# Kernel tuning notes

Hardware: AMD Instinct MI355X
Metric: run time of the kernel (lower is better)

## Reference

```python
import jax, jax.numpy as jnp
import numpy as np

N = 50000   # nodes
E = 800000  # edges (avg degree 16)
D = 96      # feature dim for all layers


def setup_inputs() -> dict:
    key = jax.random.key(0)
    ks = jax.random.split(key, 8)
    x = jax.random.normal(ks[0], (N, D), dtype=jnp.float32)
    edge_index = jax.random.randint(ks[1], (2, E), 0, N, dtype=jnp.int32)
    edge_weight = jax.random.uniform(ks[2], (E,), dtype=jnp.float32)
    batch = jnp.zeros((N,), dtype=jnp.int32)  # unused by forward, kept for signature fidelity
    s = 1.0 / np.sqrt(D)
    W1 = jax.random.normal(ks[3], (D, D), dtype=jnp.float32) * s
    b1 = jnp.zeros((D,), dtype=jnp.float32)
    W2 = jax.random.normal(ks[4], (D, D), dtype=jnp.float32) * s
    b2 = jnp.zeros((D,), dtype=jnp.float32)
    return {"x": x, "edge_index": edge_index, "edge_weight": edge_weight,
            "batch": batch, "W1": W1, "b1": b1, "W2": W2, "b2": b2}


def gcn_conv(x, row, col, ew, W, b):
    """PyG GCNConv: add self-loops (weight 1), symmetric normalization,
    linear transform then weighted scatter-add aggregation at target (col)."""
    n = x.shape[0]
    h = x @ W  # [N, D_out]
    # degree includes self-loop weight 1.0
    deg = jax.ops.segment_sum(ew, col, num_segments=n) + 1.0
    dinv = jnp.where(deg > 0, jax.lax.rsqrt(deg), 0.0)
    norm = dinv[row] * ew * dinv[col]                      # [E]
    agg = jax.ops.segment_sum(h[row] * norm[:, None], col, num_segments=n)
    agg = agg + h * (dinv * dinv)[:, None]                 # self-loop messages
    return agg + b


def reference(x, edge_index, edge_weight, batch, W1, b1, W2, b2):
    row, col = edge_index[0], edge_index[1]
    # layer 1: conv -> relu (dropout p=0.0 is a no-op)
    h = jax.nn.relu(gcn_conv(x, row, col, edge_weight, W1, b1))
    # layer 2
    h = jax.nn.relu(gcn_conv(h, row, col, edge_weight, W2, b2))
    return h
```

## Files before the change

### kernel.cpp

```cpp
#include <hip/hip_runtime.h>
#include <hip/hip_fp16.h>

#define DIM 96
#define DIM4 (DIM/4)
#define CAP 64

typedef _Float16 f16x8 __attribute__((ext_vector_type(8)));
typedef float    f32x4 __attribute__((ext_vector_type(4)));

#define WSCALE 4194304.0f


#define PREP_BLOCKS 256

__global__ __launch_bounds__(256) void prep_kernel(unsigned long long* __restrict__ pdeg,
                                                   const float* __restrict__ W1,
                                                   const float* __restrict__ W2,
                                                   _Float16* __restrict__ Bt1,
                                                   _Float16* __restrict__ Bt2, int n) {
    for (int i = blockIdx.x * 256 + threadIdx.x; i < n; i += PREP_BLOCKS * 256)
        pdeg[i] = 0ULL;
    int i = blockIdx.x * 256 + threadIdx.x;
    if (i < DIM * DIM) {
        int c = i / DIM, k = i - c * DIM;
        Bt1[i] = (_Float16)W1[k * DIM + c];
        Bt2[i] = (_Float16)W2[k * DIM + c];
    }
}


__global__ void edge_pack_kernel(const int* __restrict__ col, const float* __restrict__ ew,
                                 unsigned long long* __restrict__ pdeg,
                                 unsigned* __restrict__ spack,
                                 const int* __restrict__ row, int e) {
    int i = blockIdx.x * blockDim.x + threadIdx.x;
    if (i < e) {
        float w = ew[i];
        unsigned q = (unsigned)(w * WSCALE + 0.5f);
        unsigned long long old =
            atomicAdd(&pdeg[col[i]], (1ULL << 32) | (unsigned long long)q);
        unsigned rk = (unsigned)(old >> 32);
        if (rk < CAP) {
            unsigned hb = (unsigned)__half_as_ushort(__float2half_rn(w));
            spack[(size_t)col[i] * CAP + rk] = ((unsigned)row[i] << 16) | hb;
        }
    }
}


__global__ void dinv_kernel(const unsigned long long* __restrict__ pdeg,
                            float* __restrict__ dinv, int* __restrict__ cnt, int n) {
    int i = blockIdx.x * blockDim.x + threadIdx.x;
    if (i < n) {
        unsigned long long p = pdeg[i];
        int c = (int)(p >> 32);
        cnt[i] = c > CAP ? CAP : c;
        float deg = 1.0f + (float)(p & 0xffffffffULL) * (1.0f / WSCALE);
        dinv[i] = rsqrtf(deg);
    }
}


template<bool A_IS_F32>
__global__ __launch_bounds__(256) void gemm_mfma_kernel(const void* __restrict__ Av,
                                                        const _Float16* __restrict__ Bt,
                                                        const float* __restrict__ dinv,
                                                        _Float16* __restrict__ H, int n) {
    int wave = threadIdx.x >> 6;
    int lane = threadIdx.x & 63;
    int r0 = blockIdx.x * 64 + wave * 16;
    if (r0 >= n) return;

    int lrow = lane & 15;
    int lk   = (lane >> 4) << 3;
    int arow = r0 + lrow;
    if (arow > n - 1) arow = n - 1;

    const _Float16* Ah = (const _Float16*)Av;
    const float*    Af = (const float*)Av;

    f32x4 acc[6] = {};

#pragma unroll
    for (int ks = 0; ks < 3; ++ks) {
        int k0 = ks * 32 + lk;
        f16x8 a;
        if (A_IS_F32) {
            const float* ap = Af + (size_t)arow * DIM + k0;
            float4 x0 = *(const float4*)ap;
            float4 x1 = *(const float4*)(ap + 4);
            a[0] = (_Float16)x0.x; a[1] = (_Float16)x0.y;
            a[2] = (_Float16)x0.z; a[3] = (_Float16)x0.w;
            a[4] = (_Float16)x1.x; a[5] = (_Float16)x1.y;
            a[6] = (_Float16)x1.z; a[7] = (_Float16)x1.w;
        } else {
            a = *(const f16x8*)(Ah + (size_t)arow * DIM + k0);
        }
#pragma unroll
        for (int ct = 0; ct < 6; ++ct) {
            f16x8 b = *(const f16x8*)(Bt + (size_t)(ct * 16 + lrow) * DIM + k0);
            acc[ct] = __builtin_amdgcn_mfma_f32_16x16x32_f16(a, b, acc[ct], 0, 0, 0);
        }
    }

    int crow = r0 + ((lane >> 4) << 2);
    int ccol = lane & 15;
#pragma unroll
    for (int ct = 0; ct < 6; ++ct) {
#pragma unroll
        for (int j = 0; j < 4; ++j) {
            int rr = crow + j;
            if (rr < n)
                H[(size_t)rr * DIM + ct * 16 + ccol] = (_Float16)(acc[ct][j] * dinv[rr]);
        }
    }
}


#define GLN 12
#define GNPB 16

__device__ __forceinline__ float4 half4_to_float4_u2(unsigned a, unsigned b) {
    __half2 h01 = *(const __half2*)&a;
    __half2 h23 = *(const __half2*)&b;
    float2 f01 = __half22float2(h01);
    float2 f23 = __half22float2(h23);
    return make_float4(f01.x, f01.y, f23.x, f23.y);
}

__device__ __forceinline__ float wdec(unsigned e) {
    return __half2float(__ushort_as_half((unsigned short)(e & 0xffffu)));
}

template<bool OUT_F32>
__global__ __launch_bounds__(192) void gather_kernel(const int* __restrict__ cnt,
                                                     const unsigned* __restrict__ spack,
                                                     const float* __restrict__ dinv,
                                                     const __half* __restrict__ H,
                                                     const float* __restrict__ bias,
                                                     float* __restrict__ outf,
                                                     __half* __restrict__ outh, int n) {
    int ln = threadIdx.x / GLN;
    int q  = threadIdx.x - ln * GLN;
    int node = blockIdx.x * GNPB + ln;
    if (node >= n) return;

    const unsigned* seg = spack + (size_t)node * CAP;
    int nedge = cnt[node];
    float di = dinv[node];

    const uint4* Hq = (const uint4*)H;

    float4 accA = make_float4(0.f, 0.f, 0.f, 0.f);
    float4 accB = make_float4(0.f, 0.f, 0.f, 0.f);
    int p = 0;
    for (; p + 3 < nedge; p += 4) {
        unsigned e0 = seg[p];
        unsigned e1 = seg[p + 1];
        unsigned e2 = seg[p + 2];
        unsigned e3 = seg[p + 3];
        uint4 v0 = Hq[(e0 >> 16) * 12 + q];
        uint4 v1 = Hq[(e1 >> 16) * 12 + q];
        uint4 v2 = Hq[(e2 >> 16) * 12 + q];
        uint4 v3 = Hq[(e3 >> 16) * 12 + q];
        float w0 = wdec(e0), w1 = wdec(e1), w2 = wdec(e2), w3 = wdec(e3);
        float4 a0 = half4_to_float4_u2(v0.x, v0.y), b0 = half4_to_float4_u2(v0.z, v0.w);
        float4 a1 = half4_to_float4_u2(v1.x, v1.y), b1 = half4_to_float4_u2(v1.z, v1.w);
        float4 a2 = half4_to_float4_u2(v2.x, v2.y), b2 = half4_to_float4_u2(v2.z, v2.w);
        float4 a3 = half4_to_float4_u2(v3.x, v3.y), b3 = half4_to_float4_u2(v3.z, v3.w);
        accA.x = fmaf(w0, a0.x, accA.x); accA.y = fmaf(w0, a0.y, accA.y);
        accA.z = fmaf(w0, a0.z, accA.z); accA.w = fmaf(w0, a0.w, accA.w);
        accB.x = fmaf(w0, b0.x, accB.x); accB.y = fmaf(w0, b0.y, accB.y);
        accB.z = fmaf(w0, b0.z, accB.z); accB.w = fmaf(w0, b0.w, accB.w);
        accA.x = fmaf(w1, a1.x, accA.x); accA.y = fmaf(w1, a1.y, accA.y);
        accA.z = fmaf(w1, a1.z, accA.z); accA.w = fmaf(w1, a1.w, accA.w);
        accB.x = fmaf(w1, b1.x, accB.x); accB.y = fmaf(w1, b1.y, accB.y);
        accB.z = fmaf(w1, b1.z, accB.z); accB.w = fmaf(w1, b1.w, accB.w);
        accA.x = fmaf(w2, a2.x, accA.x); accA.y = fmaf(w2, a2.y, accA.y);
        accA.z = fmaf(w2, a2.z, accA.z); accA.w = fmaf(w2, a2.w, accA.w);
        accB.x = fmaf(w2, b2.x, accB.x); accB.y = fmaf(w2, b2.y, accB.y);
        accB.z = fmaf(w2, b2.z, accB.z); accB.w = fmaf(w2, b2.w, accB.w);
        accA.x = fmaf(w3, a3.x, accA.x); accA.y = fmaf(w3, a3.y, accA.y);
        accA.z = fmaf(w3, a3.z, accA.z); accA.w = fmaf(w3, a3.w, accA.w);
        accB.x = fmaf(w3, b3.x, accB.x); accB.y = fmaf(w3, b3.y, accB.y);
        accB.z = fmaf(w3, b3.z, accB.z); accB.w = fmaf(w3, b3.w, accB.w);
    }
    for (; p < nedge; ++p) {
        unsigned e0 = seg[p];
        float w0 = wdec(e0);
        uint4 v0 = Hq[(e0 >> 16) * 12 + q];
        float4 a0 = half4_to_float4_u2(v0.x, v0.y), b0 = half4_to_float4_u2(v0.z, v0.w);
        accA.x = fmaf(w0, a0.x, accA.x); accA.y = fmaf(w0, a0.y, accA.y);
        accA.z = fmaf(w0, a0.z, accA.z); accA.w = fmaf(w0, a0.w, accA.w);
        accB.x = fmaf(w0, b0.x, accB.x); accB.y = fmaf(w0, b0.y, accB.y);
        accB.z = fmaf(w0, b0.z, accB.z); accB.w = fmaf(w0, b0.w, accB.w);
    }

    uint4 hv = Hq[node * 12 + q];
    float4 hcA = half4_to_float4_u2(hv.x, hv.y);
    float4 hcB = half4_to_float4_u2(hv.z, hv.w);
    float4 bA = ((const float4*)bias)[2 * q];
    float4 bB = ((const float4*)bias)[2 * q + 1];

    float4 oA, oB;
    oA.x = fmaxf(fmaf(accA.x + hcA.x, di, bA.x), 0.0f);
    oA.y = fmaxf(fmaf(accA.y + hcA.y, di, bA.y), 0.0f);
    oA.z = fmaxf(fmaf(accA.z + hcA.z, di, bA.z), 0.0f);
    oA.w = fmaxf(fmaf(accA.w + hcA.w, di, bA.w), 0.0f);
    oB.x = fmaxf(fmaf(accB.x + hcB.x, di, bB.x), 0.0f);
    oB.y = fmaxf(fmaf(accB.y + hcB.y, di, bB.y), 0.0f);
    oB.z = fmaxf(fmaf(accB.z + hcB.z, di, bB.z), 0.0f);
    oB.w = fmaxf(fmaf(accB.w + hcB.w, di, bB.w), 0.0f);

    if (OUT_F32) {
        ((float4*)(outf + (size_t)node * DIM))[2 * q]     = oA;
        ((float4*)(outf + (size_t)node * DIM))[2 * q + 1] = oB;
    } else {
        __half2 p01 = __float22half2_rn(make_float2(oA.x, oA.y));
        __half2 p23 = __float22half2_rn(make_float2(oA.z, oA.w));
        __half2 p45 = __float22half2_rn(make_float2(oB.x, oB.y));
        __half2 p67 = __float22half2_rn(make_float2(oB.z, oB.w));
        uint4 u;
        u.x = *(const unsigned*)&p01;
        u.y = *(const unsigned*)&p23;
        u.z = *(const unsigned*)&p45;
        u.w = *(const unsigned*)&p67;
        ((uint4*)outh)[node * 12 + q] = u;
    }
}


extern "C" void kernel_launch(void* const* d_in, const int* in_sizes, int n_in,
                              void* d_out, int out_size, void* d_ws, size_t ws_size,
                              hipStream_t stream) {
    const float* x   = (const float*)d_in[0];
    const int*   ei  = (const int*)d_in[1];
    const float* ew  = (const float*)d_in[2];
    const float* W1  = (const float*)d_in[4];
    const float* b1  = (const float*)d_in[5];
    const float* W2  = (const float*)d_in[6];
    const float* b2  = (const float*)d_in[7];

    const int N = in_sizes[0] / DIM;
    const int E = in_sizes[1] / 2;
    const int* row = ei;
    const int* col = ei + E;

    char* ws = (char*)d_ws;
    size_t off = 0;
    auto alloc = [&](size_t bytes) { void* p = ws + off; off = (off + bytes + 255) & ~(size_t)255; return p; };
    unsigned long long* pdeg = (unsigned long long*)alloc((size_t)N * 8);
    float* dinv   = (float*)alloc((size_t)N * 4);
    int*   cnt    = (int*)  alloc((size_t)N * 4);
    unsigned* spack = (unsigned*)alloc((size_t)N * CAP * 4);
    _Float16* A   = (_Float16*)alloc((size_t)N * DIM * 2);
    _Float16* y1h = (_Float16*)alloc((size_t)N * DIM * 2);
    _Float16* Bt1 = (_Float16*)alloc((size_t)DIM * DIM * 2);
    _Float16* Bt2 = (_Float16*)alloc((size_t)DIM * DIM * 2);
    float* out    = (float*)d_out;

    dim3 blk(256);
    int gN  = (N + 255) / 256;
    int gE  = (E + 255) / 256;
    int gMM = (N + 63) / 64;
    int gG  = (N + GNPB - 1) / GNPB;

    prep_kernel<<<PREP_BLOCKS, blk, 0, stream>>>(pdeg, W1, W2, Bt1, Bt2, N);
    edge_pack_kernel<<<gE, blk, 0, stream>>>(col, ew, pdeg, spack, row, E);
    dinv_kernel<<<gN, blk, 0, stream>>>(pdeg, dinv, cnt, N);

    gemm_mfma_kernel<true><<<gMM, blk, 0, stream>>>(x, Bt1, dinv, A, N);
    gather_kernel<false><<<gG, 192, 0, stream>>>(cnt, spack, dinv, (const __half*)A, b1,
                                                 nullptr, (__half*)y1h, N);

    gemm_mfma_kernel<false><<<gMM, blk, 0, stream>>>(y1h, Bt2, dinv, A, N);
    gather_kernel<true><<<gG, 192, 0, stream>>>(cnt, spack, dinv, (const __half*)A, b2,
                                                out, nullptr, N);
}
```

Measured before the change: 146.4 us.

## Fuse layer-1 gather with layer-2 GEMM via LDS and drop dinv kernel

Removes the dinv/cnt kernel and computes the degree normalization inline from the packed degree word in each consumer. Fuses the layer-1 neighbor gather with the layer-2 MFMA GEMM: each 192-thread block aggregates 48 nodes into shared memory in fp16, then three waves multiply those rows by W2. This saves two launches and the global write and read of the intermediate activations. In exchange, the fused kernel has a barrier and more LDS per block, which may reduce gather occupancy and overlap.

```diff
diff --git a/kernel.cpp b/kernel.cpp
--- a/kernel.cpp
+++ b/kernel.cpp
@@ -2,7 +2,6 @@
 #include <hip/hip_fp16.h>
 
 #define DIM 96
-#define DIM4 (DIM/4)
 #define CAP 64
 
 typedef _Float16 f16x8 __attribute__((ext_vector_type(8)));
@@ -48,77 +47,9 @@
 }
 
 
-__global__ void dinv_kernel(const unsigned long long* __restrict__ pdeg,
-                            float* __restrict__ dinv, int* __restrict__ cnt, int n) {
-    int i = blockIdx.x * blockDim.x + threadIdx.x;
-    if (i < n) {
-        unsigned long long p = pdeg[i];
-        int c = (int)(p >> 32);
-        cnt[i] = c > CAP ? CAP : c;
-        float deg = 1.0f + (float)(p & 0xffffffffULL) * (1.0f / WSCALE);
-        dinv[i] = rsqrtf(deg);
-    }
-}
-
-
-template<bool A_IS_F32>
-__global__ __launch_bounds__(256) void gemm_mfma_kernel(const void* __restrict__ Av,
-                                                        const _Float16* __restrict__ Bt,
-                                                        const float* __restrict__ dinv,
-                                                        _Float16* __restrict__ H, int n) {
-    int wave = threadIdx.x >> 6;
-    int lane = threadIdx.x & 63;
-    int r0 = blockIdx.x * 64 + wave * 16;
-    if (r0 >= n) return;
-
-    int lrow = lane & 15;
-    int lk   = (lane >> 4) << 3;
-    int arow = r0 + lrow;
-    if (arow > n - 1) arow = n - 1;
-
-    const _Float16* Ah = (const _Float16*)Av;
-    const float*    Af = (const float*)Av;
-
-    f32x4 acc[6] = {};
-
-#pragma unroll
-    for (int ks = 0; ks < 3; ++ks) {
-        int k0 = ks * 32 + lk;
-        f16x8 a;
-        if (A_IS_F32) {
-            const float* ap = Af + (size_t)arow * DIM + k0;
-            float4 x0 = *(const float4*)ap;
-            float4 x1 = *(const float4*)(ap + 4);
-            a[0] = (_Float16)x0.x; a[1] = (_Float16)x0.y;
-            a[2] = (_Float16)x0.z; a[3] = (_Float16)x0.w;
-            a[4] = (_Float16)x1.x; a[5] = (_Float16)x1.y;
-            a[6] = (_Float16)x1.z; a[7] = (_Float16)x1.w;
-        } else {
-            a = *(const f16x8*)(Ah + (size_t)arow * DIM + k0);
-        }
-#pragma unroll
-        for (int ct = 0; ct < 6; ++ct) {
-            f16x8 b = *(const f16x8*)(Bt + (size_t)(ct * 16 + lrow) * DIM + k0);
-            acc[ct] = __builtin_amdgcn_mfma_f32_16x16x32_f16(a, b, acc[ct], 0, 0, 0);
-        }
-    }
-
-    int crow = r0 + ((lane >> 4) << 2);
-    int ccol = lane & 15;
-#pragma unroll
-    for (int ct = 0; ct < 6; ++ct) {
-#pragma unroll
-        for (int j = 0; j < 4; ++j) {
-            int rr = crow + j;
-            if (rr < n)
-                H[(size_t)rr * DIM + ct * 16 + ccol] = (_Float16)(acc[ct][j] * dinv[rr]);
-        }
-    }
-}
-
-
-#define GLN 12
-#define GNPB 16
+__device__ __forceinline__ float pdeg_dinv(unsigned long long p) {
+    return rsqrtf(1.0f + (float)(p & 0xffffffffULL) * (1.0f / WSCALE));
+}
 
 __device__ __forceinline__ float4 half4_to_float4_u2(unsigned a, unsigned b) {
     __half2 h01 = *(const __half2*)&a;
@@ -132,22 +63,213 @@
     return __half2float(__ushort_as_half((unsigned short)(e & 0xffffu)));
 }
 
-template<bool OUT_F32>
-__global__ __launch_bounds__(192) void gather_kernel(const int* __restrict__ cnt,
-                                                     const unsigned* __restrict__ spack,
-                                                     const float* __restrict__ dinv,
-                                                     const __half* __restrict__ H,
-                                                     const float* __restrict__ bias,
-                                                     float* __restrict__ outf,
-                                                     __half* __restrict__ outh, int n) {
+
+__global__ __launch_bounds__(256) void gemm1_kernel(const float* __restrict__ X,
+                                                    const _Float16* __restrict__ Bt,
+                                                    const unsigned long long* __restrict__ pdeg,
+                                                    _Float16* __restrict__ H, int n) {
+    int wave = threadIdx.x >> 6;
+    int lane = threadIdx.x & 63;
+    int r0 = blockIdx.x * 64 + wave * 16;
+    if (r0 >= n) return;
+
+    int lrow = lane & 15;
+    int lk   = (lane >> 4) << 3;
+    int arow = r0 + lrow;
+    if (arow > n - 1) arow = n - 1;
+
+    f32x4 acc[6] = {};
+#pragma unroll
+    for (int ks = 0; ks < 3; ++ks) {
+        int k0 = ks * 32 + lk;
+        const float* ap = X + (size_t)arow * DIM + k0;
+        float4 x0 = *(const float4*)ap;
+        float4 x1 = *(const float4*)(ap + 4);
+        f16x8 a;
+        a[0] = (_Float16)x0.x; a[1] = (_Float16)x0.y;
+        a[2] = (_Float16)x0.z; a[3] = (_Float16)x0.w;
+        a[4] = (_Float16)x1.x; a[5] = (_Float16)x1.y;
+        a[6] = (_Float16)x1.z; a[7] = (_Float16)x1.w;
+#pragma unroll
+        for (int ct = 0; ct < 6; ++ct) {
+            f16x8 b = *(const f16x8*)(Bt + (size_t)(ct * 16 + lrow) * DIM + k0);
+            acc[ct] = __builtin_amdgcn_mfma_f32_16x16x32_f16(a, b, acc[ct], 0, 0, 0);
+        }
+    }
+
+    int crow = r0 + ((lane >> 4) << 2);
+    int ccol = lane & 15;
+    float dv[4];
+#pragma unroll
+    for (int j = 0; j < 4; ++j) {
+        int rr = crow + j;
+        dv[j] = (rr < n) ? pdeg_dinv(pdeg[rr]) : 0.f;
+    }
+#pragma unroll
+    for (int ct = 0; ct < 6; ++ct) {
+#pragma unroll
+        for (int j = 0; j < 4; ++j) {
+            int rr = crow + j;
+            if (rr < n)
+                H[(size_t)rr * DIM + ct * 16 + ccol] = (_Float16)(acc[ct][j] * dv[j]);
+        }
+    }
+}
+
+
+__global__ __launch_bounds__(192) void fused_g1g2_kernel(
+        const unsigned long long* __restrict__ pdeg,
+        const unsigned* __restrict__ spack,
+        const __half* __restrict__ H1,
+        const float* __restrict__ bias1,
+        const _Float16* __restrict__ Bt2,
+        _Float16* __restrict__ H2, int n) {
+    __shared__ uint4 y1s[48][13];
+
+    int tid = threadIdx.x;
+    int ln = tid / 12;
+    int q  = tid - ln * 12;
+    const uint4* Hq = (const uint4*)H1;
+
+#pragma unroll
+    for (int r = 0; r < 3; ++r) {
+        int nl = r * 16 + ln;
+        int node = blockIdx.x * 48 + nl;
+        uint4 u = make_uint4(0u, 0u, 0u, 0u);
+        if (node < n) {
+            unsigned long long pd = pdeg[node];
+            int nedge = (int)(pd >> 32); if (nedge > CAP) nedge = CAP;
+            float di = pdeg_dinv(pd);
+            const unsigned* seg = spack + (size_t)node * CAP;
+
+            float4 accA = make_float4(0.f, 0.f, 0.f, 0.f);
+            float4 accB = make_float4(0.f, 0.f, 0.f, 0.f);
+            int p = 0;
+            for (; p + 3 < nedge; p += 4) {
+                unsigned e0 = seg[p], e1 = seg[p + 1], e2 = seg[p + 2], e3 = seg[p + 3];
+                uint4 v0 = Hq[(e0 >> 16) * 12 + q];
+                uint4 v1 = Hq[(e1 >> 16) * 12 + q];
+                uint4 v2 = Hq[(e2 >> 16) * 12 + q];
+                uint4 v3 = Hq[(e3 >> 16) * 12 + q];
+                float w0 = wdec(e0), w1 = wdec(e1), w2 = wdec(e2), w3 = wdec(e3);
+                float4 a0 = half4_to_float4_u2(v0.x, v0.y), b0 = half4_to_float4_u2(v0.z, v0.w);
+                float4 a1 = half4_to_float4_u2(v1.x, v1.y), b1 = half4_to_float4_u2(v1.z, v1.w);
+                float4 a2 = half4_to_float4_u2(v2.x, v2.y), b2 = half4_to_float4_u2(v2.z, v2.w);
+                float4 a3 = half4_to_float4_u2(v3.x, v3.y), b3 = half4_to_float4_u2(v3.z, v3.w);
+                accA.x = fmaf(w0, a0.x, accA.x); accA.y = fmaf(w0, a0.y, accA.y);
+                accA.z = fmaf(w0, a0.z, accA.z); accA.w = fmaf(w0, a0.w, accA.w);
+                accB.x = fmaf(w0, b0.x, accB.x); accB.y = fmaf(w0, b0.y, accB.y);
+                accB.z = fmaf(w0, b0.z, accB.z); accB.w = fmaf(w0, b0.w, accB.w);
+                accA.x = fmaf(w1, a1.x, accA.x); accA.y = fmaf(w1, a1.y, accA.y);
+                accA.z = fmaf(w1, a1.z, accA.z); accA.w = fmaf(w1, a1.w, accA.w);
+                accB.x = fmaf(w1, b1.x, accB.x); accB.y = fmaf(w1, b1.y, accB.y);
+                accB.z = fmaf(w1, b1.z, accB.z); accB.w = fmaf(w1, b1.w, accB.w);
+                accA.x = fmaf(w2, a2.x, accA.x); accA.y = fmaf(w2, a2.y, accA.y);
+                accA.z = fmaf(w2, a2.z, accA.z); accA.w = fmaf(w2, a2.w, accA.w);
+                accB.x = fmaf(w2, b2.x, accB.x); accB.y = fmaf(w2, b2.y, accB.y);
+                accB.z = fmaf(w2, b2.z, accB.z); accB.w = fmaf(w2, b2.w, accB.w);
+                accA.x = fmaf(w3, a3.x, accA.x); accA.y = fmaf(w3, a3.y, accA.y);
+                accA.z = fmaf(w3, a3.z, accA.z); accA.w = fmaf(w3, a3.w, accA.w);
+                accB.x = fmaf(w3, b3.x, accB.x); accB.y = fmaf(w3, b3.y, accB.y);
+                accB.z = fmaf(w3, b3.z, accB.z); accB.w = fmaf(w3, b3.w, accB.w);
+            }
+            for (; p < nedge; ++p) {
+                unsigned e0 = seg[p];
+                float w0 = wdec(e0);
+                uint4 v0 = Hq[(e0 >> 16) * 12 + q];
+                float4 a0 = half4_to_float4_u2(v0.x, v0.y), b0 = half4_to_float4_u2(v0.z, v0.w);
+                accA.x = fmaf(w0, a0.x, accA.x); accA.y = fmaf(w0, a0.y, accA.y);
+                accA.z = fmaf(w0, a0.z, accA.z); accA.w = fmaf(w0, a0.w, accA.w);
+                accB.x = fmaf(w0, b0.x, accB.x); accB.y = fmaf(w0, b0.y, accB.y);
+                accB.z = fmaf(w0, b0.z, accB.z); accB.w = fmaf(w0, b0.w, accB.w);
+            }
+
+            uint4 hv = Hq[node * 12 + q];
+            float4 hcA = half4_to_float4_u2(hv.x, hv.y);
+            float4 hcB = half4_to_float4_u2(hv.z, hv.w);
+            float4 bA = ((const float4*)bias1)[2 * q];
+            float4 bB = ((const float4*)bias1)[2 * q + 1];
+
+            float4 oA, oB;
+            oA.x = fmaxf(fmaf(accA.x + hcA.x, di, bA.x), 0.0f);
+            oA.y = fmaxf(fmaf(accA.y + hcA.y, di, bA.y), 0.0f);
+            oA.z = fmaxf(fmaf(accA.z + hcA.z, di, bA.z), 0.0f);
+            oA.w = fmaxf(fmaf(accA.w + hcA.w, di, bA.w), 0.0f);
+            oB.x = fmaxf(fmaf(accB.x + hcB.x, di, bB.x), 0.0f);
+            oB.y = fmaxf(fmaf(accB.y + hcB.y, di, bB.y), 0.0f);
+            oB.z = fmaxf(fmaf(accB.z + hcB.z, di, bB.z), 0.0f);
+            oB.w = fmaxf(fmaf(accB.w + hcB.w, di, bB.w), 0.0f);
+
+            __half2 p01 = __float22half2_rn(make_float2(oA.x, oA.y));
+            __half2 p23 = __float22half2_rn(make_float2(oA.z, oA.w));
+            __half2 p45 = __float22half2_rn(make_float2(oB.x, oB.y));
+            __half2 p67 = __float22half2_rn(make_float2(oB.z, oB.w));
+            u.x = *(const unsigned*)&p01;
+            u.y = *(const unsigned*)&p23;
+            u.z = *(const unsigned*)&p45;
+            u.w = *(const unsigned*)&p67;
+        }
+        y1s[nl][q] = u;
+    }
+    __syncthreads();
+
+    int wave = tid >> 6;
+    int lane = tid & 63;
+    int lrow = lane & 15;
+    int ck   = lane >> 4;
+    int r0 = blockIdx.x * 48 + wave * 16;
+    if (r0 >= n) return;
+
+    f32x4 acc[6] = {};
+#pragma unroll
+    for (int ks = 0; ks < 3; ++ks) {
+        uint4 av = y1s[wave * 16 + lrow][ks * 4 + ck];
+        f16x8 a = *(const f16x8*)&av;
+        int k0 = ks * 32 + ck * 8;
+#pragma unroll
+        for (int ct = 0; ct < 6; ++ct) {
+            f16x8 b = *(const f16x8*)(Bt2 + (size_t)(ct * 16 + lrow) * DIM + k0);
+            acc[ct] = __builtin_amdgcn_mfma_f32_16x16x32_f16(a, b, acc[ct], 0, 0, 0);
+        }
+    }
+
+    int crow = r0 + (ck << 2);
+    int ccol = lane & 15;
+    float dv[4];
+#pragma unroll
+    for (int j = 0; j < 4; ++j) {
+        int rr = crow + j;
+        dv[j] = (rr < n) ? pdeg_dinv(pdeg[rr]) : 0.f;
+    }
+#pragma unroll
+    for (int ct = 0; ct < 6; ++ct) {
+#pragma unroll
+        for (int j = 0; j < 4; ++j) {
+            int rr = crow + j;
+            if (rr < n)
+                H2[(size_t)rr * DIM + ct * 16 + ccol] = (_Float16)(acc[ct][j] * dv[j]);
+        }
+    }
+}
+
+
+#define GLN 12
+#define GNPB 16
+
+__global__ __launch_bounds__(192) void gather2_kernel(const unsigned long long* __restrict__ pdeg,
+                                                      const unsigned* __restrict__ spack,
+                                                      const __half* __restrict__ H,
+                                                      const float* __restrict__ bias,
+                                                      float* __restrict__ outf, int n) {
     int ln = threadIdx.x / GLN;
     int q  = threadIdx.x - ln * GLN;
     int node = blockIdx.x * GNPB + ln;
     if (node >= n) return;
 
+    unsigned long long pd = pdeg[node];
+    int nedge = (int)(pd >> 32); if (nedge > CAP) nedge = CAP;
+    float di = pdeg_dinv(pd);
     const unsigned* seg = spack + (size_t)node * CAP;
-    int nedge = cnt[node];
-    float di = dinv[node];
 
     const uint4* Hq = (const uint4*)H;
 
@@ -155,10 +277,7 @@
     float4 accB = make_float4(0.f, 0.f, 0.f, 0.f);
     int p = 0;
     for (; p + 3 < nedge; p += 4) {
-        unsigned e0 = seg[p];
-        unsigned e1 = seg[p + 1];
-        unsigned e2 = seg[p + 2];
-        unsigned e3 = seg[p + 3];
+        unsigned e0 = seg[p], e1 = seg[p + 1], e2 = seg[p + 2], e3 = seg[p + 3];
         uint4 v0 = Hq[(e0 >> 16) * 12 + q];
         uint4 v1 = Hq[(e1 >> 16) * 12 + q];
         uint4 v2 = Hq[(e2 >> 16) * 12 + q];
@@ -212,21 +331,8 @@
     oB.z = fmaxf(fmaf(accB.z + hcB.z, di, bB.z), 0.0f);
     oB.w = fmaxf(fmaf(accB.w + hcB.w, di, bB.w), 0.0f);
 
-    if (OUT_F32) {
-        ((float4*)(outf + (size_t)node * DIM))[2 * q]     = oA;
-        ((float4*)(outf + (size_t)node * DIM))[2 * q + 1] = oB;
-    } else {
-        __half2 p01 = __float22half2_rn(make_float2(oA.x, oA.y));
-        __half2 p23 = __float22half2_rn(make_float2(oA.z, oA.w));
-        __half2 p45 = __float22half2_rn(make_float2(oB.x, oB.y));
-        __half2 p67 = __float22half2_rn(make_float2(oB.z, oB.w));
-        uint4 u;
-        u.x = *(const unsigned*)&p01;
-        u.y = *(const unsigned*)&p23;
-        u.z = *(const unsigned*)&p45;
-        u.w = *(const unsigned*)&p67;
-        ((uint4*)outh)[node * 12 + q] = u;
-    }
+    ((float4*)(outf + (size_t)node * DIM))[2 * q]     = oA;
+    ((float4*)(outf + (size_t)node * DIM))[2 * q + 1] = oB;
 }
 
 
@@ -250,30 +356,22 @@
     size_t off = 0;
     auto alloc = [&](size_t bytes) { void* p = ws + off; off = (off + bytes + 255) & ~(size_t)255; return p; };
     unsigned long long* pdeg = (unsigned long long*)alloc((size_t)N * 8);
-    float* dinv   = (float*)alloc((size_t)N * 4);
-    int*   cnt    = (int*)  alloc((size_t)N * 4);
     unsigned* spack = (unsigned*)alloc((size_t)N * CAP * 4);
     _Float16* A   = (_Float16*)alloc((size_t)N * DIM * 2);
-    _Float16* y1h = (_Float16*)alloc((size_t)N * DIM * 2);
+    _Float16* B   = (_Float16*)alloc((size_t)N * DIM * 2);
     _Float16* Bt1 = (_Float16*)alloc((size_t)DIM * DIM * 2);
     _Float16* Bt2 = (_Float16*)alloc((size_t)DIM * DIM * 2);
     float* out    = (float*)d_out;
 
     dim3 blk(256);
-    int gN  = (N + 255) / 256;
     int gE  = (E + 255) / 256;
     int gMM = (N + 63) / 64;
+    int gF  = (N + 47) / 48;
     int gG  = (N + GNPB - 1) / GNPB;
 
     prep_kernel<<<PREP_BLOCKS, blk, 0, stream>>>(pdeg, W1, W2, Bt1, Bt2, N);
     edge_pack_kernel<<<gE, blk, 0, stream>>>(col, ew, pdeg, spack, row, E);
-    dinv_kernel<<<gN, blk, 0, stream>>>(pdeg, dinv, cnt, N);
-
-    gemm_mfma_kernel<true><<<gMM, blk, 0, stream>>>(x, Bt1, dinv, A, N);
-    gather_kernel<false><<<gG, 192, 0, stream>>>(cnt, spack, dinv, (const __half*)A, b1,
-                                                 nullptr, (__half*)y1h, N);
-
-    gemm_mfma_kernel<false><<<gMM, blk, 0, stream>>>(y1h, Bt2, dinv, A, N);
-    gather_kernel<true><<<gG, 192, 0, stream>>>(cnt, spack, dinv, (const __half*)A, b2,
-                                                out, nullptr, N);
-}
+    gemm1_kernel<<<gMM, blk, 0, stream>>>(x, Bt1, pdeg, A, N);
+    fused_g1g2_kernel<<<gF, 192, 0, stream>>>(pdeg, spack, (const __half*)A, b1, Bt2, B, N);
+    gather2_kernel<<<gG, 192, 0, stream>>>(pdeg, spack, (const __half*)B, b2, out, N);
+}
```

Result: faster. 131.7 us (-10.0%).
